# Kernel tuning notes

Hardware: AMD Instinct MI355X
Metric: run time of the kernel (lower is better)

## Reference

```python
import jax, jax.numpy as jnp
import numpy as np
from jax import lax

B, V, M, C, CM, D = 48, 16, 32, 48, 8, 128
VOCAB_V, VOCAB_M, OUT = 2000, 1000, 256


def setup_inputs() -> dict:
    key = jax.random.key(0)
    ks = jax.random.split(key, 22)
    s = 0.1  # keep GRU gates out of saturation
    return {
        "visit_ids": jax.random.randint(ks[0], (3, B, V, C), 0, VOCAB_V),
        "mon_ids": jax.random.randint(ks[1], (4, B, V, M, CM), 0, VOCAB_M),
        "weight_vals": jax.random.uniform(ks[2], (B, V)),
        "age_vals": jax.random.uniform(ks[3], (B, V)),
        "emb_visit": jax.random.normal(ks[4], (3, VOCAB_V, D)) * s,
        "emb_mon": jax.random.normal(ks[5], (4, VOCAB_M, D)) * s,
        "mgru_Wih": jax.random.normal(ks[6], (5, 3 * D, D)) * s,
        "mgru_Whh": jax.random.normal(ks[7], (5, 3 * D, D)) * s,
        "mgru_bih": jax.random.normal(ks[8], (5, 3 * D)) * s,
        "mgru_bhh": jax.random.normal(ks[9], (5, 3 * D)) * s,
        "vgru_Wih": jax.random.normal(ks[10], (7, 3 * D, D)) * s,
        "vgru_Whh": jax.random.normal(ks[11], (7, 3 * D, D)) * s,
        "vgru_bih": jax.random.normal(ks[12], (7, 3 * D)) * s,
        "vgru_bhh": jax.random.normal(ks[13], (7, 3 * D)) * s,
        "fc_weight_w": jax.random.normal(ks[14], (D, 1)) * s,
        "fc_weight_b": jax.random.normal(ks[15], (D,)) * s,
        "fc_age_w": jax.random.normal(ks[16], (D, 1)) * s,
        "fc_age_b": jax.random.normal(ks[17], (D,)) * s,
        "fc_out_w": jax.random.normal(ks[18], (OUT, 7 * D)) * s,
        "fc_out_b": jax.random.normal(ks[19], (OUT,)) * s,
    }


def gru_last(x, Wih, Whh, bih, bhh):
    """torch.nn.GRU(batch_first=True), return final hidden [N, D]."""
    xi = jnp.einsum('ntd,ed->nte', x, Wih) + bih  # [N, T, 3D] input projections
    h0 = jnp.zeros((x.shape[0], Whh.shape[1]), x.dtype)

    def step(h, gi):
        gh = h @ Whh.T + bhh
        ir, iz, inn = jnp.split(gi, 3, axis=-1)
        hr, hz, hn = jnp.split(gh, 3, axis=-1)
        r = jax.nn.sigmoid(ir + hr)
        z = jax.nn.sigmoid(iz + hz)
        n = jnp.tanh(inn + r * hn)
        return (1.0 - z) * n + z * h, None

    hT, _ = lax.scan(step, h0, jnp.swapaxes(xi, 0, 1))
    return hT


def reference(visit_ids, mon_ids, weight_vals, age_vals, emb_visit, emb_mon,
              mgru_Wih, mgru_Whh, mgru_bih, mgru_bhh,
              vgru_Wih, vgru_Whh, vgru_bih, vgru_bhh,
              fc_weight_w, fc_weight_b, fc_age_w, fc_age_b,
              fc_out_w, fc_out_b):
    # padding_idx=0 -> zero embedding row (dropout in eval mode = identity)
    ev = emb_visit.at[:, 0].set(0.0)
    em = emb_mon.at[:, 0].set(0.0)

    # visit-event embedding-bag: sum over code dim -> [B, V, D] per feature
    visit_origin = [jnp.sum(ev[k][visit_ids[k]], axis=2) for k in range(3)]

    def run_stream(t, mi, vi):
        # monitor-level GRU over M, then visit-level GRU over V
        h1 = gru_last(t, mgru_Wih[mi], mgru_Whh[mi], mgru_bih[mi], mgru_bhh[mi])
        h2 = gru_last(h1.reshape(B, V, D),
                      vgru_Wih[vi], vgru_Whh[vi], vgru_bih[vi], vgru_bhh[vi])
        return h2  # [B, D]

    # output slots in dict-insertion order: lab_item, cond, proc, drug, inj_item, weight, age
    slots = [None] * 7
    for p in range(2):  # (lab_item, lab_value), (inj_item, inj_value)
        # elementwise item*value embedding, summed over codes -> [B*V, M, D]
        mon = jnp.sum(em[2 * p][mon_ids[2 * p]] * em[2 * p + 1][mon_ids[2 * p + 1]],
                      axis=3).reshape(B * V, M, D)
        slots[0 if p == 0 else 4] = run_stream(mon, p, p)
        for k in range(3):  # visit features repeated along monitor dim
            t = jnp.broadcast_to(visit_origin[k][:, :, None, :],
                                 (B, V, M, D)).reshape(B * V, M, D)
            h = run_stream(t, 2 + k, 2 + k)
            slots[1 + k] = h if slots[1 + k] is None else slots[1 + k] + h

    # weight / age: Linear(1->D), zero-mask, visit-level GRU
    for vals, w, b, vi, slot in ((weight_vals, fc_weight_w, fc_weight_b, 5, 5),
                                 (age_vals, fc_age_w, fc_age_b, 6, 6)):
        xf = vals.reshape(-1, 1)
        h = (xf @ w.T + b) * (xf != 0)
        slots[slot] = gru_last(h.reshape(B, V, D),
                               vgru_Wih[vi], vgru_Whh[vi], vgru_bih[vi], vgru_bhh[vi])

    patient_emb = jnp.concatenate(slots, axis=-1)  # [B, 7D]
    return jax.nn.relu(patient_emb) @ fc_out_w.T + fc_out_b
```

## Files before the change

kernel.cpp:

```cpp
#include <hip/hip_runtime.h>
#include <stdint.h>


typedef unsigned short u16;
typedef uint32_t u32;
typedef short bf8 __attribute__((ext_vector_type(8)));
typedef float f4 __attribute__((ext_vector_type(4)));

static __device__ __forceinline__ float bf2f(u16 b){ u32 u=((u32)b)<<16; float f; __builtin_memcpy(&f,&u,4); return f; }
static __device__ __forceinline__ u16 f2bf(float f){ u32 u; __builtin_memcpy(&u,&f,4); u32 r=(u+0x7fffu+((u>>16)&1u))>>16; return (u16)r; }
static __device__ __forceinline__ float bflo(u32 u){ u32 x=u<<16; float f; __builtin_memcpy(&f,&x,4); return f; }
static __device__ __forceinline__ float bfhi(u32 u){ u32 x=u&0xffff0000u; float f; __builtin_memcpy(&f,&x,4); return f; }
static __device__ __forceinline__ f4 mfma16(bf8 a, bf8 b, f4 c){ return __builtin_amdgcn_mfma_f32_16x16x32_bf16(a,b,c,0,0,0); }

#if __has_builtin(__builtin_amdgcn_exp2f)
static __device__ __forceinline__ float fexp2(float x){ return __builtin_amdgcn_exp2f(x); }
#else
static __device__ __forceinline__ float fexp2(float x){ float r; asm volatile("v_exp_f32 %0, %1" : "=v"(r) : "v"(x)); return r; }
#endif
#if __has_builtin(__builtin_amdgcn_rcpf)
static __device__ __forceinline__ float frcp(float x){ return __builtin_amdgcn_rcpf(x); }
#else
static __device__ __forceinline__ float frcp(float x){ float r; asm volatile("v_rcp_f32 %0, %1" : "=v"(r) : "v"(x)); return r; }
#endif

#define LOG2E 1.44269504089f
static __device__ __forceinline__ float sigm(float x){ return frcp(1.0f + fexp2(-LOG2E*x)); }
static __device__ __forceinline__ float tanh_f(float x){ return 1.0f - 2.0f*frcp(1.0f + fexp2((2.0f*LOG2E)*x)); }

__global__ __launch_bounds__(256) void k_prep(const float* __restrict__ s0, const float* __restrict__ s1,
                                              const float* __restrict__ s2, const float* __restrict__ s3,
                                              const float* __restrict__ s4,
                                              u16* __restrict__ d0, u16* __restrict__ d1,
                                              u16* __restrict__ d2, u16* __restrict__ d3,
                                              u16* __restrict__ d4){
  int y = blockIdx.y;
  const float* src = y==0?s0 : y==1?s1 : y==2?s2 : y==3?s3 : s4;
  u16* dst         = y==0?d0 : y==1?d1 : y==2?d2 : y==3?d3 : d4;
  int n4 = (y<2 ? 245760 : y<4 ? 344064 : 512000) >> 2;
  int i = blockIdx.x*256 + threadIdx.x;
  if (i < n4){
    float4 v = *(const float4*)(src + (size_t)i*4);
    ushort4 o = { f2bf(v.x), f2bf(v.y), f2bf(v.z), f2bf(v.w) };
    *(ushort4*)(dst + (size_t)i*4) = o;
  }
}

__global__ __launch_bounds__(128) void k_front(const int* __restrict__ vids,
                                               const float* __restrict__ embv,
                                               const float* __restrict__ wv, const float* __restrict__ av,
                                               const float* __restrict__ ww, const float* __restrict__ wb,
                                               const float* __restrict__ aw, const float* __restrict__ ab,
                                               u16* __restrict__ vis_org, u16* __restrict__ hin2T){
  __shared__ int ids[48];
  int y = blockIdx.y, row = blockIdx.x, d = threadIdx.x;
  if (y < 3){
    if (d < 48) ids[d] = vids[((size_t)y*768 + row)*48 + d];
    __syncthreads();
    const float* eb = embv + (size_t)y*2000*128;
    float acc = 0.f;
    #pragma unroll 4
    for (int c = 0; c < 48; ++c){ int id = ids[c]; if (id) acc += eb[(size_t)id*128 + d]; }
    vis_org[((size_t)y*768 + row)*128 + d] = f2bf(acc);
  } else {
    int sidx = y - 3;
    const float* vals = sidx ? av : wv;
    const float* wgt  = sidx ? aw : ww;
    const float* bias = sidx ? ab : wb;
    float v = vals[row];
    float h = (v != 0.f) ? (v * wgt[d] + bias[d]) : 0.f;
    int b = row >> 4, vv = row & 15;
    hin2T[((size_t)(5+sidx)*768 + (size_t)vv*48 + b)*128 + d] = f2bf(h);
  }
}

__global__ __launch_bounds__(256) void k_embed_mon(const int* __restrict__ mids,
                                                   const u16* __restrict__ embm_b,
                                                   u16* __restrict__ mon_xT){
  int p = blockIdx.y;
  int rid = threadIdx.x >> 5, lane32 = threadIdx.x & 31, d0 = lane32*4;
  __shared__ int ids[8][16];
  if (threadIdx.x < 128){
    int rr = threadIdx.x >> 4, c = threadIdx.x & 15;
    int f = 2*p + (c>>3), cm = c & 7;
    ids[rr][c] = mids[((size_t)f*24576 + (size_t)blockIdx.x*8 + rr)*8 + cm];
  }
  __syncthreads();
  const u16* e1 = embm_b + (size_t)(2*p)*1000*128;
  const u16* e2 = embm_b + (size_t)(2*p+1)*1000*128;
  float a0=0.f,a1=0.f,a2=0.f,a3=0.f;
  #pragma unroll
  for (int c = 0; c < 8; ++c){
    int i1 = ids[rid][c], i2 = ids[rid][8+c];
    if (i1 && i2){
      uint2 a = *(const uint2*)(e1 + (size_t)i1*128 + d0);
      uint2 b = *(const uint2*)(e2 + (size_t)i2*128 + d0);
      a0 += bflo(a.x)*bflo(b.x); a1 += bfhi(a.x)*bfhi(b.x);
      a2 += bflo(a.y)*bflo(b.y); a3 += bfhi(a.y)*bfhi(b.y);
    }
  }
  size_t nm = (size_t)blockIdx.x*8 + rid;
  int bv = (int)(nm >> 5), m = (int)(nm & 31);
  ushort4 o = { f2bf(a0), f2bf(a1), f2bf(a2), f2bf(a3) };
  *(ushort4*)(mon_xT + (size_t)p*24576*128 + ((size_t)m*768 + bv)*128 + d0) = o;
}


#define BARRIER() asm volatile("s_waitcnt lgkmcnt(0)\n\ts_barrier" ::: "memory")

#define ALOAD(D, tt) { int t_=(tt); if (t_>=T) t_=0; \
  const u16* p_ = ap + (size_t)t_*rstride; \
  D[0]=*(const bf8*)(p_); D[1]=*(const bf8*)(p_+32); \
  D[2]=*(const bf8*)(p_+64); D[3]=*(const bf8*)(p_+96); }

#define GIMM(G0,G1,G2,D) { \
  f4 t0_={biv[0],biv[0],biv[0],biv[0]}; G0=t0_; \
  f4 t1_={biv[1],biv[1],biv[1],biv[1]}; G1=t1_; \
  f4 t2_={biv[2],biv[2],biv[2],biv[2]}; G2=t2_; \
  G0=mfma16(D[0],wfi[0][0],G0); G0=mfma16(D[1],wfi[0][1],G0); \
  G0=mfma16(D[2],wfi[0][2],G0); G0=mfma16(D[3],wfi[0][3],G0); \
  G1=mfma16(D[0],wfi[1][0],G1); G1=mfma16(D[1],wfi[1][1],G1); \
  G1=mfma16(D[2],wfi[1][2],G1); G1=mfma16(D[3],wfi[1][3],G1); \
  G2=mfma16(D[0],wfi[2][0],G2); G2=mfma16(D[1],wfi[2][1],G2); \
  G2=mfma16(D[2],wfi[2][2],G2); G2=mfma16(D[3],wfi[2][3],G2); }

#define GHRD() \
  bf8 hf0_=*(const bf8*)&hlds[cur][lr][lq*8]; \
  bf8 hf1_=*(const bf8*)&hlds[cur][lr][32+lq*8]; \
  bf8 hf2_=*(const bf8*)&hlds[cur][lr][64+lq*8]; \
  bf8 hf3_=*(const bf8*)&hlds[cur][lr][96+lq*8]; \
  f4 a0_={bhv[0],bhv[0],bhv[0],bhv[0]}; \
  f4 a1_={bhv[1],bhv[1],bhv[1],bhv[1]}; \
  f4 a2_={bhv[2],bhv[2],bhv[2],bhv[2]}; \
  a0_=mfma16(hf0_,wfh[0][0],a0_); a0_=mfma16(hf1_,wfh[0][1],a0_); \
  a0_=mfma16(hf2_,wfh[0][2],a0_); a0_=mfma16(hf3_,wfh[0][3],a0_); \
  a1_=mfma16(hf0_,wfh[1][0],a1_); a1_=mfma16(hf1_,wfh[1][1],a1_); \
  a1_=mfma16(hf2_,wfh[1][2],a1_); a1_=mfma16(hf3_,wfh[1][3],a1_); \
  a2_=mfma16(hf0_,wfh[2][0],a2_); a2_=mfma16(hf1_,wfh[2][1],a2_); \
  a2_=mfma16(hf2_,wfh[2][2],a2_); a2_=mfma16(hf3_,wfh[2][3],a2_);

#define GATES(G0,G1,G2) { int nxt_=cur^1; \
  _Pragma("unroll") \
  for (int r=0;r<4;++r){ \
    float rr_=sigm(G0[r]+a0_[r]); \
    float zz_=sigm(G1[r]+a1_[r]); \
    float nn_=tanh_f(G2[r]+rr_*a2_[r]); \
    float hv_=(1.0f-zz_)*nn_+zz_*hp[r]; hp[r]=hv_; \
    hlds[nxt_][lq*4+r][w*16+lr]=f2bf(hv_); } \
  BARRIER(); cur=nxt_; }

#define STEP0(G0,G1,G2) { \
  f4 a0_={bhv[0],bhv[0],bhv[0],bhv[0]}; \
  f4 a1_={bhv[1],bhv[1],bhv[1],bhv[1]}; \
  f4 a2_={bhv[2],bhv[2],bhv[2],bhv[2]}; \
  GATES(G0,G1,G2); }

#define STEPB(G0,G1,G2,SN,tt) { \
  GHRD(); \
  GATES(G0,G1,G2); \
  if ((tt)+2 < T){ GIMM(G0,G1,G2,SN); } \
  ALOAD(SN,(tt)+4); }

__global__ __launch_bounds__(512, 2) void k_gru(int mode,
    const u16* __restrict__ Asrc, const u16* __restrict__ Asrc2,
    const u16* __restrict__ Wih, const float* __restrict__ bih,
    const u16* __restrict__ Whh, const float* __restrict__ bhh,
    u16* __restrict__ hout, int T){
  int s = blockIdx.y, g = blockIdx.x;
  const u16* A; size_t rstride; u16* ho; int widx;
  if (mode == 0){
    if (s < 2){ A = Asrc + (size_t)s*24576*128; rstride = 768*128; }
    else      { A = Asrc2 + (size_t)(s-2)*768*128; rstride = 0; }
    widx = s;
    int slot = (0x32140u >> (4*s)) & 15;
    ho = hout + (size_t)slot*768*128;
  } else {
    A = Asrc + (size_t)s*768*128; rstride = 48*128;
    widx = (0x6514320u >> (4*s)) & 15;
    ho = hout + (size_t)s*48*128;
  }
  const u16* Wi = Wih + (size_t)widx*384*128;
  const u16* Wh = Whh + (size_t)widx*384*128;
  const float* bi = bih + (size_t)widx*384;
  const float* bh = bhh + (size_t)widx*384;

  int w = threadIdx.x >> 6, l = threadIdx.x & 63;
  int lr = l & 15, lq = l >> 4;

  bf8 wfi[3][4], wfh[3][4]; float biv[3], bhv[3];
  #pragma unroll
  for (int j = 0; j < 3; ++j){
    int colb = (w + 8*j)*16;
    const u16* wpi = Wi + (size_t)(colb + lr)*128 + lq*8;
    const u16* wph = Wh + (size_t)(colb + lr)*128 + lq*8;
    #pragma unroll
    for (int kt = 0; kt < 4; ++kt){
      wfi[j][kt] = *(const bf8*)(wpi + kt*32);
      wfh[j][kt] = *(const bf8*)(wph + kt*32);
    }
    biv[j] = bi[colb + lr];
    bhv[j] = bh[colb + lr];
  }

  const u16* ap = A + (size_t)(g*16 + lr)*128 + lq*8;
  __shared__ u16 hlds[2][16][132];
  float hp[4] = {0.f,0.f,0.f,0.f};
  int cur = 0;

  if (rstride){
    bf8 S0[4], S1[4];
    f4 gE0,gE1,gE2, gO0,gO1,gO2;
    ALOAD(S0,0); ALOAD(S1,1);
    GIMM(gE0,gE1,gE2,S0); ALOAD(S0,2);
    GIMM(gO0,gO1,gO2,S1); ALOAD(S1,3);
    STEP0(gE0,gE1,gE2);
    GIMM(gE0,gE1,gE2,S0); ALOAD(S0,4);
    STEPB(gO0,gO1,gO2,S1,1);
    for (int t = 2; t < T; t += 2){
      STEPB(gE0,gE1,gE2,S0,t);
      STEPB(gO0,gO1,gO2,S1,t+1);
    }
  } else {
    bf8 S0[4];
    f4 gE0,gE1,gE2;
    ALOAD(S0,0);
    GIMM(gE0,gE1,gE2,S0);
    STEP0(gE0,gE1,gE2);
    for (int t = 1; t < T; ++t){
      GHRD();
      GATES(gE0,gE1,gE2);
    }
  }

  if (mode == 0){
    #pragma unroll
    for (int r = 0; r < 4; ++r)
      ho[((size_t)(lq*4+r)*48 + g)*128 + w*16 + lr] = f2bf(hp[r]);
  } else {
    #pragma unroll
    for (int r = 0; r < 4; ++r)
      ho[((size_t)(g*16 + lq*4 + r))*128 + w*16 + lr] = f2bf(hp[r]);
  }
}

__global__ __launch_bounds__(256) void k_final(const u16* __restrict__ h2,
                                               const float* __restrict__ W,
                                               const float* __restrict__ Bias,
                                               float* __restrict__ out){
  int b = blockIdx.x, t = threadIdx.x;
  __shared__ float emb[896];
  for (int i = t; i < 896; i += 256){
    int j = i >> 7, d = i & 127;
    float v = bf2f(h2[((size_t)j*48 + b)*128 + d]);
    if (j >= 1 && j <= 3) v *= 2.0f;
    emb[i] = fmaxf(v, 0.f);
  }
  __syncthreads();
  float acc = Bias[t];
  const float* wp = W + (size_t)t*896;
  for (int i = 0; i < 896; i += 8){
    float4 w0 = *(const float4*)(wp + i);
    float4 w1 = *(const float4*)(wp + i + 4);
    acc += w0.x*emb[i]   + w0.y*emb[i+1] + w0.z*emb[i+2] + w0.w*emb[i+3];
    acc += w1.x*emb[i+4] + w1.y*emb[i+5] + w1.z*emb[i+6] + w1.w*emb[i+7];
  }
  out[(size_t)b*256 + t] = acc;
}

extern "C" void kernel_launch(void* const* d_in, const int* in_sizes, int n_in,
                              void* d_out, int out_size, void* d_ws, size_t ws_size,
                              hipStream_t stream){
  const int*   visit_ids   = (const int*)d_in[0];
  const int*   mon_ids     = (const int*)d_in[1];
  const float* weight_vals = (const float*)d_in[2];
  const float* age_vals    = (const float*)d_in[3];
  const float* emb_visit   = (const float*)d_in[4];
  const float* emb_mon     = (const float*)d_in[5];
  const float* mgru_Wih    = (const float*)d_in[6];
  const float* mgru_Whh    = (const float*)d_in[7];
  const float* mgru_bih    = (const float*)d_in[8];
  const float* mgru_bhh    = (const float*)d_in[9];
  const float* vgru_Wih    = (const float*)d_in[10];
  const float* vgru_Whh    = (const float*)d_in[11];
  const float* vgru_bih    = (const float*)d_in[12];
  const float* vgru_bhh    = (const float*)d_in[13];
  const float* fc_w_w      = (const float*)d_in[14];
  const float* fc_w_b      = (const float*)d_in[15];
  const float* fc_a_w      = (const float*)d_in[16];
  const float* fc_a_b      = (const float*)d_in[17];
  const float* fc_out_w    = (const float*)d_in[18];
  const float* fc_out_b    = (const float*)d_in[19];

  char* ws = (char*)d_ws;
  size_t o = 0;
  u16* mWih_b  = (u16*)(ws+o); o += 5ull*384*128*2;
  u16* mWhh_b  = (u16*)(ws+o); o += 5ull*384*128*2;
  u16* vWih_b  = (u16*)(ws+o); o += 7ull*384*128*2;
  u16* vWhh_b  = (u16*)(ws+o); o += 7ull*384*128*2;
  u16* embm_b  = (u16*)(ws+o); o += 4ull*1000*128*2;
  u16* mon_xT  = (u16*)(ws+o); o += 2ull*24576*128*2;
  u16* vis_org = (u16*)(ws+o); o += 3ull*768*128*2;
  u16* hin2T   = (u16*)(ws+o); o += 7ull*768*128*2;
  u16* h2      = (u16*)(ws+o); o += 7ull*48*128*2;

  k_prep<<<dim3(500,5), 256, 0, stream>>>(mgru_Wih, mgru_Whh, vgru_Wih, vgru_Whh, emb_mon,
                                          mWih_b, mWhh_b, vWih_b, vWhh_b, embm_b);
  k_front<<<dim3(768,5), 128, 0, stream>>>(visit_ids, emb_visit,
                                           weight_vals, age_vals, fc_w_w, fc_w_b, fc_a_w, fc_a_b,
                                           vis_org, hin2T);
  k_embed_mon<<<dim3(3072,2), 256, 0, stream>>>(mon_ids, embm_b, mon_xT);
  k_gru<<<dim3(48,5), 512, 0, stream>>>(0, mon_xT, vis_org,
                                        mWih_b, mgru_bih, mWhh_b, mgru_bhh, hin2T, 32);
  k_gru<<<dim3(3,7), 512, 0, stream>>>(1, hin2T, (const u16*)0,
                                       vWih_b, vgru_bih, vWhh_b, vgru_bhh, h2, 16);
  k_final<<<48, 256, 0, stream>>>(h2, fc_out_w, fc_out_b, (float*)d_out);
}
```

Before: 132.9 us.

## Merge front-end kernels and overlap weight/age GRUs with monitor GRUs

Merges the visit-bag, weight/age projection and monitor-bag kernels into one k_bags launch, and folds visit-embedding bf16 conversion into a single flattened k_prep. The weight and age visit-level GRUs now run as extra blocks in the first GRU launch, in parallel with the monitor GRUs, so the second GRU launch only handles five streams. Inside each GRU step the barrier moves after the next input projection and prefetch, so that work can overlap the LDS synchronisation. The aim is fewer launches and a shorter serial chain. The cost is that visit embeddings are now summed from bf16 rather than fp32, which adds rounding error.

After: 142.2 us. 7.0% more time.

```diff
diff --git a/kernel.cpp b/kernel.cpp
--- a/kernel.cpp
+++ b/kernel.cpp
@@ -23,106 +23,111 @@
 #else
 static __device__ __forceinline__ float frcp(float x){ float r; asm volatile("v_rcp_f32 %0, %1" : "=v"(r) : "v"(x)); return r; }
 #endif
-
 #define LOG2E 1.44269504089f
 static __device__ __forceinline__ float sigm(float x){ return frcp(1.0f + fexp2(-LOG2E*x)); }
 static __device__ __forceinline__ float tanh_f(float x){ return 1.0f - 2.0f*frcp(1.0f + fexp2((2.0f*LOG2E)*x)); }
 
-__global__ __launch_bounds__(256) void k_prep(const float* __restrict__ s0, const float* __restrict__ s1,
-                                              const float* __restrict__ s2, const float* __restrict__ s3,
-                                              const float* __restrict__ s4,
-                                              u16* __restrict__ d0, u16* __restrict__ d1,
-                                              u16* __restrict__ d2, u16* __restrict__ d3,
-                                              u16* __restrict__ d4){
+__global__ __launch_bounds__(256) void k_prep(
+    const float* __restrict__ s0, const float* __restrict__ s1,
+    const float* __restrict__ s2, const float* __restrict__ s3,
+    const float* __restrict__ s4, const float* __restrict__ s5,
+    u16* __restrict__ d0, u16* __restrict__ d1, u16* __restrict__ d2,
+    u16* __restrict__ d3, u16* __restrict__ d4, u16* __restrict__ d5){
+  int i = blockIdx.x*256 + threadIdx.x;
+  const float* s; u16* d; int off;
+  if      (i < 61440)  { s=s0; d=d0; off=i; }
+  else if (i < 122880) { s=s1; d=d1; off=i-61440; }
+  else if (i < 208896) { s=s2; d=d2; off=i-122880; }
+  else if (i < 294912) { s=s3; d=d3; off=i-208896; }
+  else if (i < 422912) { s=s4; d=d4; off=i-294912; }
+  else if (i < 614912) { s=s5; d=d5; off=i-422912; }
+  else return;
+  float4 v = *(const float4*)(s + (size_t)off*4);
+  ushort4 o = { f2bf(v.x), f2bf(v.y), f2bf(v.z), f2bf(v.w) };
+  *(ushort4*)(d + (size_t)off*4) = o;
+}
+
+__global__ __launch_bounds__(256) void k_bags(const int* __restrict__ vids, const int* __restrict__ mids,
+    const u16* __restrict__ embv_b, const u16* __restrict__ embm_b,
+    const float* __restrict__ wv, const float* __restrict__ av,
+    const float* __restrict__ ww, const float* __restrict__ wb,
+    const float* __restrict__ aw, const float* __restrict__ ab,
+    u16* __restrict__ mon_xT, u16* __restrict__ vis_org, u16* __restrict__ hin2T){
   int y = blockIdx.y;
-  const float* src = y==0?s0 : y==1?s1 : y==2?s2 : y==3?s3 : s4;
-  u16* dst         = y==0?d0 : y==1?d1 : y==2?d2 : y==3?d3 : d4;
-  int n4 = (y<2 ? 245760 : y<4 ? 344064 : 512000) >> 2;
-  int i = blockIdx.x*256 + threadIdx.x;
-  if (i < n4){
-    float4 v = *(const float4*)(src + (size_t)i*4);
-    ushort4 o = { f2bf(v.x), f2bf(v.y), f2bf(v.z), f2bf(v.w) };
-    *(ushort4*)(dst + (size_t)i*4) = o;
-  }
-}
-
-__global__ __launch_bounds__(128) void k_front(const int* __restrict__ vids,
-                                               const float* __restrict__ embv,
-                                               const float* __restrict__ wv, const float* __restrict__ av,
-                                               const float* __restrict__ ww, const float* __restrict__ wb,
-                                               const float* __restrict__ aw, const float* __restrict__ ab,
-                                               u16* __restrict__ vis_org, u16* __restrict__ hin2T){
-  __shared__ int ids[48];
-  int y = blockIdx.y, row = blockIdx.x, d = threadIdx.x;
-  if (y < 3){
-    if (d < 48) ids[d] = vids[((size_t)y*768 + row)*48 + d];
+  if (y < 2){
+    int p = y;
+    int rid = threadIdx.x >> 5, lane32 = threadIdx.x & 31, d0 = lane32*4;
+    __shared__ int ids[8][16];
+    if (threadIdx.x < 128){
+      int rr = threadIdx.x >> 4, c = threadIdx.x & 15;
+      int f = 2*p + (c>>3), cm = c & 7;
+      ids[rr][c] = mids[((size_t)f*24576 + (size_t)blockIdx.x*8 + rr)*8 + cm];
+    }
     __syncthreads();
-    const float* eb = embv + (size_t)y*2000*128;
-    float acc = 0.f;
-    #pragma unroll 4
-    for (int c = 0; c < 48; ++c){ int id = ids[c]; if (id) acc += eb[(size_t)id*128 + d]; }
-    vis_org[((size_t)y*768 + row)*128 + d] = f2bf(acc);
+    const u16* e1 = embm_b + (size_t)(2*p)*1000*128;
+    const u16* e2 = embm_b + (size_t)(2*p+1)*1000*128;
+    float a0=0.f,a1=0.f,a2=0.f,a3=0.f;
+    #pragma unroll
+    for (int c = 0; c < 8; ++c){
+      int i1 = ids[rid][c], i2 = ids[rid][8+c];
+      if (i1 && i2){
+        uint2 a = *(const uint2*)(e1 + (size_t)i1*128 + d0);
+        uint2 b = *(const uint2*)(e2 + (size_t)i2*128 + d0);
+        a0 += bflo(a.x)*bflo(b.x); a1 += bfhi(a.x)*bfhi(b.x);
+        a2 += bflo(a.y)*bflo(b.y); a3 += bfhi(a.y)*bfhi(b.y);
+      }
+    }
+    size_t nm = (size_t)blockIdx.x*8 + rid;
+    int bv = (int)(nm >> 5), m = (int)(nm & 31);
+    ushort4 o = { f2bf(a0), f2bf(a1), f2bf(a2), f2bf(a3) };
+    *(ushort4*)(mon_xT + (size_t)p*24576*128 + ((size_t)m*768 + bv)*128 + d0) = o;
   } else {
-    int sidx = y - 3;
-    const float* vals = sidx ? av : wv;
-    const float* wgt  = sidx ? aw : ww;
-    const float* bias = sidx ? ab : wb;
-    float v = vals[row];
-    float h = (v != 0.f) ? (v * wgt[d] + bias[d]) : 0.f;
-    int b = row >> 4, vv = row & 15;
-    hin2T[((size_t)(5+sidx)*768 + (size_t)vv*48 + b)*128 + d] = f2bf(h);
-  }
-}
-
-__global__ __launch_bounds__(256) void k_embed_mon(const int* __restrict__ mids,
-                                                   const u16* __restrict__ embm_b,
-                                                   u16* __restrict__ mon_xT){
-  int p = blockIdx.y;
-  int rid = threadIdx.x >> 5, lane32 = threadIdx.x & 31, d0 = lane32*4;
-  __shared__ int ids[8][16];
-  if (threadIdx.x < 128){
-    int rr = threadIdx.x >> 4, c = threadIdx.x & 15;
-    int f = 2*p + (c>>3), cm = c & 7;
-    ids[rr][c] = mids[((size_t)f*24576 + (size_t)blockIdx.x*8 + rr)*8 + cm];
-  }
-  __syncthreads();
-  const u16* e1 = embm_b + (size_t)(2*p)*1000*128;
-  const u16* e2 = embm_b + (size_t)(2*p+1)*1000*128;
-  float a0=0.f,a1=0.f,a2=0.f,a3=0.f;
-  #pragma unroll
-  for (int c = 0; c < 8; ++c){
-    int i1 = ids[rid][c], i2 = ids[rid][8+c];
-    if (i1 && i2){
-      uint2 a = *(const uint2*)(e1 + (size_t)i1*128 + d0);
-      uint2 b = *(const uint2*)(e2 + (size_t)i2*128 + d0);
-      a0 += bflo(a.x)*bflo(b.x); a1 += bfhi(a.x)*bfhi(b.x);
-      a2 += bflo(a.y)*bflo(b.y); a3 += bfhi(a.y)*bfhi(b.y);
-    }
-  }
-  size_t nm = (size_t)blockIdx.x*8 + rid;
-  int bv = (int)(nm >> 5), m = (int)(nm & 31);
-  ushort4 o = { f2bf(a0), f2bf(a1), f2bf(a2), f2bf(a3) };
-  *(ushort4*)(mon_xT + (size_t)p*24576*128 + ((size_t)m*768 + bv)*128 + d0) = o;
+    int x = blockIdx.x;
+    int sub = threadIdx.x >> 7, d = threadIdx.x & 127;
+    if (x < 1152){
+      __shared__ int ids[2][48];
+      int row = x*2 + sub;
+      int k = row / 768, bv = row - k*768;
+      if (d < 48) ids[sub][d] = vids[((size_t)k*768 + bv)*48 + d];
+      __syncthreads();
+      const u16* eb = embv_b + (size_t)k*2000*128;
+      float acc = 0.f;
+      #pragma unroll 4
+      for (int c = 0; c < 48; ++c){ int id = ids[sub][c]; if (id) acc += bf2f(eb[(size_t)id*128 + d]); }
+      vis_org[((size_t)k*768 + bv)*128 + d] = f2bf(acc);
+    } else if (x < 1920){
+      int grow = (x - 1152)*2 + sub;
+      int sidx = grow >= 768 ? 1 : 0;
+      int row = grow - sidx*768;
+      const float* vals = sidx ? av : wv;
+      const float* wgt  = sidx ? aw : ww;
+      const float* bias = sidx ? ab : wb;
+      float v = vals[row];
+      float h = (v != 0.f) ? (v * wgt[d] + bias[d]) : 0.f;
+      int b = row >> 4, vv = row & 15;
+      hin2T[((size_t)(5+sidx)*768 + (size_t)vv*48 + b)*128 + d] = f2bf(h);
+    }
+  }
 }
 
 
 #define BARRIER() asm volatile("s_waitcnt lgkmcnt(0)\n\ts_barrier" ::: "memory")
 
-#define ALOAD(D, tt) { int t_=(tt); if (t_>=T) t_=0; \
+#define ALOAD(S, tt) { int t_=(tt); if (t_>=T) t_=0; \
   const u16* p_ = ap + (size_t)t_*rstride; \
-  D[0]=*(const bf8*)(p_); D[1]=*(const bf8*)(p_+32); \
-  D[2]=*(const bf8*)(p_+64); D[3]=*(const bf8*)(p_+96); }
-
-#define GIMM(G0,G1,G2,D) { \
+  S[0]=*(const bf8*)(p_); S[1]=*(const bf8*)(p_+32); \
+  S[2]=*(const bf8*)(p_+64); S[3]=*(const bf8*)(p_+96); }
+
+#define GIMM(G0,G1,G2,S) { \
   f4 t0_={biv[0],biv[0],biv[0],biv[0]}; G0=t0_; \
   f4 t1_={biv[1],biv[1],biv[1],biv[1]}; G1=t1_; \
   f4 t2_={biv[2],biv[2],biv[2],biv[2]}; G2=t2_; \
-  G0=mfma16(D[0],wfi[0][0],G0); G0=mfma16(D[1],wfi[0][1],G0); \
-  G0=mfma16(D[2],wfi[0][2],G0); G0=mfma16(D[3],wfi[0][3],G0); \
-  G1=mfma16(D[0],wfi[1][0],G1); G1=mfma16(D[1],wfi[1][1],G1); \
-  G1=mfma16(D[2],wfi[1][2],G1); G1=mfma16(D[3],wfi[1][3],G1); \
-  G2=mfma16(D[0],wfi[2][0],G2); G2=mfma16(D[1],wfi[2][1],G2); \
-  G2=mfma16(D[2],wfi[2][2],G2); G2=mfma16(D[3],wfi[2][3],G2); }
+  G0=mfma16(S[0],wfi[0][0],G0); G0=mfma16(S[1],wfi[0][1],G0); \
+  G0=mfma16(S[2],wfi[0][2],G0); G0=mfma16(S[3],wfi[0][3],G0); \
+  G1=mfma16(S[0],wfi[1][0],G1); G1=mfma16(S[1],wfi[1][1],G1); \
+  G1=mfma16(S[2],wfi[1][2],G1); G1=mfma16(S[3],wfi[1][3],G1); \
+  G2=mfma16(S[0],wfi[2][0],G2); G2=mfma16(S[1],wfi[2][1],G2); \
+  G2=mfma16(S[2],wfi[2][2],G2); G2=mfma16(S[3],wfi[2][3],G2); }
 
 #define GHRD() \
   bf8 hf0_=*(const bf8*)&hlds[cur][lr][lq*8]; \
@@ -139,50 +144,49 @@
   a2_=mfma16(hf0_,wfh[2][0],a2_); a2_=mfma16(hf1_,wfh[2][1],a2_); \
   a2_=mfma16(hf2_,wfh[2][2],a2_); a2_=mfma16(hf3_,wfh[2][3],a2_);
 
-#define GATES(G0,G1,G2) { int nxt_=cur^1; \
+#define GATES_NB(G0,G1,G2) { int nxt_=cur^1; \
   _Pragma("unroll") \
   for (int r=0;r<4;++r){ \
     float rr_=sigm(G0[r]+a0_[r]); \
     float zz_=sigm(G1[r]+a1_[r]); \
     float nn_=tanh_f(G2[r]+rr_*a2_[r]); \
     float hv_=(1.0f-zz_)*nn_+zz_*hp[r]; hp[r]=hv_; \
-    hlds[nxt_][lq*4+r][w*16+lr]=f2bf(hv_); } \
-  BARRIER(); cur=nxt_; }
-
-#define STEP0(G0,G1,G2) { \
-  f4 a0_={bhv[0],bhv[0],bhv[0],bhv[0]}; \
-  f4 a1_={bhv[1],bhv[1],bhv[1],bhv[1]}; \
-  f4 a2_={bhv[2],bhv[2],bhv[2],bhv[2]}; \
-  GATES(G0,G1,G2); }
+    hlds[nxt_][lq*4+r][w*16+lr]=f2bf(hv_); } }
 
 #define STEPB(G0,G1,G2,SN,tt) { \
   GHRD(); \
-  GATES(G0,G1,G2); \
+  GATES_NB(G0,G1,G2); \
   if ((tt)+2 < T){ GIMM(G0,G1,G2,SN); } \
-  ALOAD(SN,(tt)+4); }
-
-__global__ __launch_bounds__(512, 2) void k_gru(int mode,
-    const u16* __restrict__ Asrc, const u16* __restrict__ Asrc2,
-    const u16* __restrict__ Wih, const float* __restrict__ bih,
-    const u16* __restrict__ Whh, const float* __restrict__ bhh,
-    u16* __restrict__ hout, int T){
+  ALOAD(SN,(tt)+4); \
+  BARRIER(); cur ^= 1; }
+
+__global__ __launch_bounds__(512, 2) void k_gru(int phase,
+    const u16* __restrict__ mon_xT, const u16* __restrict__ vis_org,
+    u16* __restrict__ hin2T, u16* __restrict__ h2,
+    const u16* __restrict__ mWih, const float* __restrict__ mbih,
+    const u16* __restrict__ mWhh, const float* __restrict__ mbhh,
+    const u16* __restrict__ vWih, const float* __restrict__ vbih,
+    const u16* __restrict__ vWhh, const float* __restrict__ vbhh){
   int s = blockIdx.y, g = blockIdx.x;
-  const u16* A; size_t rstride; u16* ho; int widx;
-  if (mode == 0){
-    if (s < 2){ A = Asrc + (size_t)s*24576*128; rstride = 768*128; }
-    else      { A = Asrc2 + (size_t)(s-2)*768*128; rstride = 0; }
-    widx = s;
+  const u16* A; size_t rstride; int T, oMode; u16* ho;
+  const u16 *Wi, *Wh; const float *bi2, *bh2;
+  if (phase == 0 && s < 5){
+    T = 32; oMode = 0;
+    if (s < 2){ A = mon_xT + (size_t)s*24576*128; rstride = 768*128; }
+    else      { A = vis_org + (size_t)(s-2)*768*128; rstride = 0; }
+    Wi = mWih + (size_t)s*49152; Wh = mWhh + (size_t)s*49152;
+    bi2 = mbih + (size_t)s*384;  bh2 = mbhh + (size_t)s*384;
     int slot = (0x32140u >> (4*s)) & 15;
-    ho = hout + (size_t)slot*768*128;
+    ho = hin2T + (size_t)slot*768*128;
   } else {
-    A = Asrc + (size_t)s*768*128; rstride = 48*128;
-    widx = (0x6514320u >> (4*s)) & 15;
-    ho = hout + (size_t)s*48*128;
-  }
-  const u16* Wi = Wih + (size_t)widx*384*128;
-  const u16* Wh = Whh + (size_t)widx*384*128;
-  const float* bi = bih + (size_t)widx*384;
-  const float* bh = bhh + (size_t)widx*384;
+    if (g >= 3) return;
+    T = 16; oMode = 1;
+    A = hin2T + (size_t)s*768*128; rstride = 48*128;
+    int vi = (0x6514320u >> (4*s)) & 15;
+    Wi = vWih + (size_t)vi*49152; Wh = vWhh + (size_t)vi*49152;
+    bi2 = vbih + (size_t)vi*384;  bh2 = vbhh + (size_t)vi*384;
+    ho = h2 + (size_t)s*48*128;
+  }
 
   int w = threadIdx.x >> 6, l = threadIdx.x & 63;
   int lr = l & 15, lq = l >> 4;
@@ -198,8 +202,8 @@
       wfi[j][kt] = *(const bf8*)(wpi + kt*32);
       wfh[j][kt] = *(const bf8*)(wph + kt*32);
     }
-    biv[j] = bi[colb + lr];
-    bhv[j] = bh[colb + lr];
+    biv[j] = bi2[colb + lr];
+    bhv[j] = bh2[colb + lr];
   }
 
   const u16* ap = A + (size_t)(g*16 + lr)*128 + lq*8;
@@ -213,8 +217,14 @@
     ALOAD(S0,0); ALOAD(S1,1);
     GIMM(gE0,gE1,gE2,S0); ALOAD(S0,2);
     GIMM(gO0,gO1,gO2,S1); ALOAD(S1,3);
-    STEP0(gE0,gE1,gE2);
-    GIMM(gE0,gE1,gE2,S0); ALOAD(S0,4);
+    {
+      f4 a0_={bhv[0],bhv[0],bhv[0],bhv[0]};
+      f4 a1_={bhv[1],bhv[1],bhv[1],bhv[1]};
+      f4 a2_={bhv[2],bhv[2],bhv[2],bhv[2]};
+      GATES_NB(gE0,gE1,gE2);
+      GIMM(gE0,gE1,gE2,S0); ALOAD(S0,4);
+      BARRIER(); cur ^= 1;
+    }
     STEPB(gO0,gO1,gO2,S1,1);
     for (int t = 2; t < T; t += 2){
       STEPB(gE0,gE1,gE2,S0,t);
@@ -225,14 +235,21 @@
     f4 gE0,gE1,gE2;
     ALOAD(S0,0);
     GIMM(gE0,gE1,gE2,S0);
-    STEP0(gE0,gE1,gE2);
+    {
+      f4 a0_={bhv[0],bhv[0],bhv[0],bhv[0]};
+      f4 a1_={bhv[1],bhv[1],bhv[1],bhv[1]};
+      f4 a2_={bhv[2],bhv[2],bhv[2],bhv[2]};
+      GATES_NB(gE0,gE1,gE2);
+      BARRIER(); cur ^= 1;
+    }
     for (int t = 1; t < T; ++t){
       GHRD();
-      GATES(gE0,gE1,gE2);
-    }
-  }
-
-  if (mode == 0){
+      GATES_NB(gE0,gE1,gE2);
+      BARRIER(); cur ^= 1;
+    }
+  }
+
+  if (oMode == 0){
     #pragma unroll
     for (int r = 0; r < 4; ++r)
       ho[((size_t)(lq*4+r)*48 + g)*128 + w*16 + lr] = f2bf(hp[r]);
@@ -298,20 +315,20 @@
   u16* vWih_b  = (u16*)(ws+o); o += 7ull*384*128*2;
   u16* vWhh_b  = (u16*)(ws+o); o += 7ull*384*128*2;
   u16* embm_b  = (u16*)(ws+o); o += 4ull*1000*128*2;
+  u16* embv_b  = (u16*)(ws+o); o += 3ull*2000*128*2;
   u16* mon_xT  = (u16*)(ws+o); o += 2ull*24576*128*2;
   u16* vis_org = (u16*)(ws+o); o += 3ull*768*128*2;
   u16* hin2T   = (u16*)(ws+o); o += 7ull*768*128*2;
   u16* h2      = (u16*)(ws+o); o += 7ull*48*128*2;
 
-  k_prep<<<dim3(500,5), 256, 0, stream>>>(mgru_Wih, mgru_Whh, vgru_Wih, vgru_Whh, emb_mon,
-                                          mWih_b, mWhh_b, vWih_b, vWhh_b, embm_b);
-  k_front<<<dim3(768,5), 128, 0, stream>>>(visit_ids, emb_visit,
-                                           weight_vals, age_vals, fc_w_w, fc_w_b, fc_a_w, fc_a_b,
-                                           vis_org, hin2T);
-  k_embed_mon<<<dim3(3072,2), 256, 0, stream>>>(mon_ids, embm_b, mon_xT);
-  k_gru<<<dim3(48,5), 512, 0, stream>>>(0, mon_xT, vis_org,
-                                        mWih_b, mgru_bih, mWhh_b, mgru_bhh, hin2T, 32);
-  k_gru<<<dim3(3,7), 512, 0, stream>>>(1, hin2T, (const u16*)0,
-                                       vWih_b, vgru_bih, vWhh_b, vgru_bhh, h2, 16);
+  k_prep<<<2402, 256, 0, stream>>>(mgru_Wih, mgru_Whh, vgru_Wih, vgru_Whh, emb_mon, emb_visit,
+                                   mWih_b, mWhh_b, vWih_b, vWhh_b, embm_b, embv_b);
+  k_bags<<<dim3(3072,3), 256, 0, stream>>>(visit_ids, mon_ids, embv_b, embm_b,
+      weight_vals, age_vals, fc_w_w, fc_w_b, fc_a_w, fc_a_b,
+      mon_xT, vis_org, hin2T);
+  k_gru<<<dim3(48,7), 512, 0, stream>>>(0, mon_xT, vis_org, hin2T, h2,
+      mWih_b, mgru_bih, mWhh_b, mgru_bhh, vWih_b, vgru_bih, vWhh_b, vgru_bhh);
+  k_gru<<<dim3(3,5), 512, 0, stream>>>(1, mon_xT, vis_org, hin2T, h2,
+      mWih_b, mgru_bih, mWhh_b, mgru_bhh, vWih_b, vgru_bih, vWhh_b, vgru_bhh);
   k_final<<<48, 256, 0, stream>>>(h2, fc_out_w, fc_out_b, (float*)d_out);
 }
```
